# Optimization experiments

Measured on AMD Instinct MI355X. Metric: run time of the kernel, lower is better.

The kernel has to match this reference:

```python
import jax, jax.numpy as jnp
import numpy as np

N_NODES = 100000
N_EDGES = 1600000
D_IN = 128
D_OUT = 128
NEG_SLOPE = 0.01  # F.leaky_relu default

def setup_inputs() -> dict:
    key = jax.random.key(0)
    k1, k2, k3, k4, k5, k6 = jax.random.split(key, 6)
    stdv = 1.0 / np.sqrt(D_OUT)
    return {
        "node_features": jax.random.normal(k1, (N_NODES, D_IN), dtype=jnp.float32),
        "edge_row": jax.random.randint(k2, (N_EDGES,), 0, N_NODES),  # dest node per edge
        "edge_col": jax.random.randint(k3, (N_EDGES,), 0, N_NODES),  # src node per edge
        "edge_val": jax.random.uniform(k4, (N_EDGES,), dtype=jnp.float32),
        "weight": jax.random.uniform(k5, (D_IN, D_OUT), dtype=jnp.float32, minval=-stdv, maxval=stdv),
        "bias": jax.random.uniform(k6, (D_OUT,), dtype=jnp.float32, minval=-stdv, maxval=stdv),
    }

def reference(node_features, edge_row, edge_col, edge_val, weight, bias):
    # x = node_features @ W  -> [N, D_OUT]
    h = node_features @ weight
    # spmm(adj, h): gather source features, scale by edge value, scatter-add to dest
    msg = edge_val[:, None] * h[edge_col]                       # [E, D_OUT]
    out = jax.ops.segment_sum(msg, edge_row, num_segments=node_features.shape[0])
    out = out + bias
    out = jnp.where(out >= 0, out, NEG_SLOPE * out)             # leaky_relu
    # dropout p=0 -> identity
    return out
```

## Files before the change

### kernel.cpp

```cpp
#include <hip/hip_runtime.h>

#define DMODEL 128
#define NEG_SLOPE 0.01f
#define NPB 64
#define NBK_MAX 1600
#define CPAD 16
#define SBLK 256
#define CAP 1536
#define OCAP 65536

typedef unsigned int uint;
typedef unsigned short ushort_t;
typedef __attribute__((ext_vector_type(8))) short short8v;
typedef __attribute__((ext_vector_type(4))) float float4v;

__device__ inline ushort_t f2bf(float f) {
    uint u = __float_as_uint(f);
    u += 0x7FFFu + ((u >> 16) & 1u);
    return (ushort_t)(u >> 16);
}

__global__ __launch_bounds__(256) void k_pre(const float* __restrict__ W,
                                             ushort_t* __restrict__ Wt,
                                             int* __restrict__ cur,
                                             int ztot) {
    const int b = blockIdx.x;
    if (b < 64) {
        const int t = b * 256 + threadIdx.x;
        const int k = t >> 7, c = t & 127;
        Wt[(size_t)c * DMODEL + k] = f2bf(W[(size_t)k * DMODEL + c]);
    } else {
        const int i = (b - 64) * 256 + threadIdx.x;
        if (i < ztot) cur[i] = 0;
    }
}

__global__ __launch_bounds__(1024) void k_fused(
        const int* __restrict__ er, const int* __restrict__ ec,
        const float* __restrict__ ev, int* __restrict__ cur,
        int* __restrict__ ocnt, int4* __restrict__ ovf,
        int2* __restrict__ packed0, int E, int NBK, int chunk,
        const float* __restrict__ X, const ushort_t* __restrict__ Wt,
        ushort_t* __restrict__ H, int N) {
    __shared__ int lh[NBK_MAX];
    __shared__ int lb[NBK_MAX];
    const int t = threadIdx.x;

    if (blockIdx.x < SBLK) {
        for (int k = t; k < NBK; k += 1024) lh[k] = 0;
        __syncthreads();
        const int s0 = blockIdx.x * chunk;
        const int s1 = min(E, s0 + chunk);
        for (int i = s0 + t * 4; i < s1; i += 4096) {
            if (i + 3 < s1) {
                int4 r = *(const int4*)(er + i);
                atomicAdd(&lh[r.x >> 6], 1);
                atomicAdd(&lh[r.y >> 6], 1);
                atomicAdd(&lh[r.z >> 6], 1);
                atomicAdd(&lh[r.w >> 6], 1);
            } else {
                for (int q = i; q < s1; ++q) atomicAdd(&lh[er[q] >> 6], 1);
            }
        }
        __syncthreads();
        for (int k = t; k < NBK; k += 1024) {
            int c = lh[k];
            lb[k] = c ? atomicAdd(&cur[k * CPAD], c) : 0;
            lh[k] = 0;
        }
        __syncthreads();
        for (int i = s0 + t * 4; i < s1; i += 4096) {
            if (i + 3 < s1) {
                int4 r = *(const int4*)(er + i);
                int4 c = *(const int4*)(ec + i);
                float4 v = *(const float4*)(ev + i);
                int bkt, rl, slot;
#define SCAT1(RR, CC, VV)                                                     \
                bkt = (RR) >> 6; rl = (RR) & 63;                              \
                slot = lb[bkt] + atomicAdd(&lh[bkt], 1);                      \
                if (slot < CAP)                                               \
                    packed0[(size_t)bkt * CAP + slot] =                       \
                        make_int2((rl << 17) | (CC), __float_as_int(VV));     \
                else {                                                        \
                    int o = atomicAdd(ocnt, 1);                               \
                    if (o < OCAP) ovf[o] = make_int4(bkt, rl, (CC), __float_as_int(VV)); \
                }
                SCAT1(r.x, c.x, v.x)
                SCAT1(r.y, c.y, v.y)
                SCAT1(r.z, c.z, v.z)
                SCAT1(r.w, c.w, v.w)
            } else {
                for (int q = i; q < s1; ++q) {
                    int rr = er[q];
                    int bkt = rr >> 6, rl = rr & 63;
                    int slot = lb[bkt] + atomicAdd(&lh[bkt], 1);
                    if (slot < CAP)
                        packed0[(size_t)bkt * CAP + slot] =
                            make_int2((rl << 17) | ec[q], __float_as_int(ev[q]));
                    else {
                        int o = atomicAdd(ocnt, 1);
                        if (o < OCAP) ovf[o] = make_int4(bkt, rl, ec[q], __float_as_int(ev[q]));
                    }
                }
            }
        }
    } else {
        const int gb = blockIdx.x - SBLK;
        const int wid = t >> 6, lane = t & 63;
        const int wrow = (gb * 16 + wid) * 16;
        if (wrow >= N) return;
        const int lr = lane & 15;
        const int kg = lane >> 4;

        const float* xrow = X + (size_t)(wrow + lr) * DMODEL + kg * 8;
        const ushort_t* wtb = Wt + (size_t)lr * DMODEL + kg * 8;

        float4v acc[8] = {};
#pragma unroll
        for (int s = 0; s < 4; ++s) {
            float4 x0 = *(const float4*)(xrow + s * 32);
            float4 x1 = *(const float4*)(xrow + s * 32 + 4);
            short8v af;
            af[0] = (short)f2bf(x0.x); af[1] = (short)f2bf(x0.y);
            af[2] = (short)f2bf(x0.z); af[3] = (short)f2bf(x0.w);
            af[4] = (short)f2bf(x1.x); af[5] = (short)f2bf(x1.y);
            af[6] = (short)f2bf(x1.z); af[7] = (short)f2bf(x1.w);
#pragma unroll
            for (int c = 0; c < 8; ++c) {
                short8v bf = *(const short8v*)(wtb + (size_t)c * 16 * DMODEL + s * 32);
                acc[c] = __builtin_amdgcn_mfma_f32_16x16x32_bf16(af, bf, acc[c], 0, 0, 0);
            }
        }
#pragma unroll
        for (int c = 0; c < 8; ++c) {
#pragma unroll
            for (int r = 0; r < 4; ++r) {
                const int row = wrow + kg * 4 + r;
                H[(size_t)row * DMODEL + c * 16 + lr] = f2bf(acc[c][r]);
            }
        }
    }
}

__global__ __launch_bounds__(256) void k_bagg2(const uint* __restrict__ Hb,
                                               const int* __restrict__ cur,
                                               const int* __restrict__ ocnt,
                                               const int4* __restrict__ ovf,
                                               const int2* __restrict__ packed0,
                                               const float* __restrict__ bias,
                                               float* __restrict__ out, int N) {
    __shared__ int2 srt[CAP];
    __shared__ int lcnt[NPB];
    __shared__ int lpref[NPB];
    __shared__ int lcur[NPB];
    const int t = threadIdx.x;
    const int b = blockIdx.x;
    if (t < NPB) { lcnt[t] = 0; lcur[t] = 0; }
    __syncthreads();

    const int cnt = cur[b * CPAD];
    const int staged = min(cnt, CAP);
    const int2* slab = packed0 + (size_t)b * CAP;

    int2 myent[6];
#pragma unroll
    for (int k = 0; k < 6; ++k) {
        const int i = t + k * 256;
        myent[k] = make_int2(0, 0);
        if (i < staged) {
            myent[k] = slab[i];
            atomicAdd(&lcnt[((uint)myent[k].x) >> 17], 1);
        }
    }
    __syncthreads();

    if (t < NPB) {
        int p = 0;
        for (int k = 0; k < t; ++k) p += lcnt[k];
        lpref[t] = p;
    }
    __syncthreads();

#pragma unroll
    for (int k = 0; k < 6; ++k) {
        const int i = t + k * 256;
        if (i < staged) {
            const int rl = ((uint)myent[k].x) >> 17;
            const int pos = lpref[rl] + atomicAdd(&lcur[rl], 1);
            srt[pos] = make_int2(myent[k].x & 0x1FFFF, myent[k].y);
        }
    }
    __syncthreads();

    const int wid = t >> 6, lane = t & 63;
    const int h = lane >> 5, sl = lane & 31;
    const float4 bv = ((const float4*)bias)[sl];
    const int oc = min(*ocnt, OCAP);

    for (int r = wid * 16; r < wid * 16 + 16; ++r) {
        const int node = b * NPB + r;
        if (node >= N) continue;
        const int m = lcnt[r], p0 = lpref[r];
        float4 acc = make_float4(0.f, 0.f, 0.f, 0.f);
        int jj = h;
        for (; jj + 6 < m; jj += 8) {
            const int2 e0 = srt[p0 + jj];
            const int2 e1 = srt[p0 + jj + 2];
            const int2 e2 = srt[p0 + jj + 4];
            const int2 e3 = srt[p0 + jj + 6];
            const uint2 g0 = ((const uint2*)(Hb + (size_t)e0.x * 64))[sl];
            const uint2 g1 = ((const uint2*)(Hb + (size_t)e1.x * 64))[sl];
            const uint2 g2 = ((const uint2*)(Hb + (size_t)e2.x * 64))[sl];
            const uint2 g3 = ((const uint2*)(Hb + (size_t)e3.x * 64))[sl];
            const float v0 = __int_as_float(e0.y);
            const float v1 = __int_as_float(e1.y);
            const float v2 = __int_as_float(e2.y);
            const float v3 = __int_as_float(e3.y);
            acc.x = fmaf(v0, __uint_as_float(g0.x << 16), acc.x);
            acc.y = fmaf(v0, __uint_as_float(g0.x & 0xffff0000u), acc.y);
            acc.z = fmaf(v0, __uint_as_float(g0.y << 16), acc.z);
            acc.w = fmaf(v0, __uint_as_float(g0.y & 0xffff0000u), acc.w);
            acc.x = fmaf(v1, __uint_as_float(g1.x << 16), acc.x);
            acc.y = fmaf(v1, __uint_as_float(g1.x & 0xffff0000u), acc.y);
            acc.z = fmaf(v1, __uint_as_float(g1.y << 16), acc.z);
            acc.w = fmaf(v1, __uint_as_float(g1.y & 0xffff0000u), acc.w);
            acc.x = fmaf(v2, __uint_as_float(g2.x << 16), acc.x);
            acc.y = fmaf(v2, __uint_as_float(g2.x & 0xffff0000u), acc.y);
            acc.z = fmaf(v2, __uint_as_float(g2.y << 16), acc.z);
            acc.w = fmaf(v2, __uint_as_float(g2.y & 0xffff0000u), acc.w);
            acc.x = fmaf(v3, __uint_as_float(g3.x << 16), acc.x);
            acc.y = fmaf(v3, __uint_as_float(g3.x & 0xffff0000u), acc.y);
            acc.z = fmaf(v3, __uint_as_float(g3.y << 16), acc.z);
            acc.w = fmaf(v3, __uint_as_float(g3.y & 0xffff0000u), acc.w);
        }
        for (; jj < m; jj += 2) {
            const int2 e0 = srt[p0 + jj];
            const uint2 g0 = ((const uint2*)(Hb + (size_t)e0.x * 64))[sl];
            const float v0 = __int_as_float(e0.y);
            acc.x = fmaf(v0, __uint_as_float(g0.x << 16), acc.x);
            acc.y = fmaf(v0, __uint_as_float(g0.x & 0xffff0000u), acc.y);
            acc.z = fmaf(v0, __uint_as_float(g0.y << 16), acc.z);
            acc.w = fmaf(v0, __uint_as_float(g0.y & 0xffff0000u), acc.w);
        }
        for (int i = 0; i < oc; ++i) {
            const int4 o4 = ovf[i];
            if (o4.x == b && o4.y == r && h == 0) {
                const float v = __int_as_float(o4.w);
                const uint2 g = ((const uint2*)(Hb + (size_t)o4.z * 64))[sl];
                acc.x = fmaf(v, __uint_as_float(g.x << 16), acc.x);
                acc.y = fmaf(v, __uint_as_float(g.x & 0xffff0000u), acc.y);
                acc.z = fmaf(v, __uint_as_float(g.y << 16), acc.z);
                acc.w = fmaf(v, __uint_as_float(g.y & 0xffff0000u), acc.w);
            }
        }
        acc.x += __shfl_xor(acc.x, 32);
        acc.y += __shfl_xor(acc.y, 32);
        acc.z += __shfl_xor(acc.z, 32);
        acc.w += __shfl_xor(acc.w, 32);
        if (h == 0) {
            float4 o;
            o.x = acc.x + bv.x; o.y = acc.y + bv.y;
            o.z = acc.z + bv.z; o.w = acc.w + bv.w;
            o.x = o.x >= 0.f ? o.x : NEG_SLOPE * o.x;
            o.y = o.y >= 0.f ? o.y : NEG_SLOPE * o.y;
            o.z = o.z >= 0.f ? o.z : NEG_SLOPE * o.z;
            o.w = o.w >= 0.f ? o.w : NEG_SLOPE * o.w;
            ((float4*)(out + (size_t)node * DMODEL))[sl] = o;
        }
    }
}

extern "C" void kernel_launch(void* const* d_in, const int* in_sizes, int n_in,
                              void* d_out, int out_size, void* d_ws, size_t ws_size,
                              hipStream_t stream) {
    const float* X    = (const float*)d_in[0];
    const int*   er   = (const int*)d_in[1];
    const int*   ec   = (const int*)d_in[2];
    const float* ev   = (const float*)d_in[3];
    const float* W    = (const float*)d_in[4];
    const float* bias = (const float*)d_in[5];
    float* out = (float*)d_out;

    const int N = in_sizes[0] / DMODEL;
    const int E = in_sizes[1];
    const int NBK = (N + NPB - 1) / NPB;

    char* ws = (char*)d_ws;
    size_t off = 0;
    auto alloc = [&](size_t bytes) {
        void* p = ws + off;
        off += (bytes + 127) & ~(size_t)127;
        return p;
    };
    ushort_t* H   = (ushort_t*)alloc((size_t)N * DMODEL * sizeof(ushort_t));
    ushort_t* Wt  = (ushort_t*)alloc((size_t)DMODEL * DMODEL * sizeof(ushort_t));
    int* cur      = (int*)alloc(((size_t)NBK * CPAD + 1) * sizeof(int));
    int* ocnt     = cur + (size_t)NBK * CPAD;
    int4* ovf     = (int4*)alloc((size_t)OCAP * sizeof(int4));
    int2* packed0 = (int2*)alloc((size_t)NBK * CAP * sizeof(int2));
    (void)ws_size;

    const int ztot = NBK * CPAD + 1;

    hipLaunchKernelGGL(k_pre, dim3(64 + (ztot + 255) / 256), dim3(256), 0, stream,
                       W, Wt, cur, ztot);

    const int chunk = ((((E + SBLK - 1) / SBLK) + 3) & ~3);
    const int gemm_blocks = (N + 255) / 256;
    hipLaunchKernelGGL(k_fused, dim3(SBLK + gemm_blocks), dim3(1024), 0, stream,
                       er, ec, ev, cur, ocnt, ovf, packed0, E, NBK, chunk,
                       X, Wt, H, N);

    hipLaunchKernelGGL(k_bagg2, dim3(NBK), dim3(256), 0, stream,
                       (const uint*)H, cur, ocnt, ovf, packed0, bias, out, N);
}
```

Measured before the change: 149.6 us.

## Split fused scatter/GEMM kernel and stage X tile through swizzled LDS

Splits the fused kernel, which ran edge bucketing and the X@W GEMM in different blocks of one launch, into a dedicated GEMM kernel and a scatter kernel. The GEMM now uses 256-thread blocks that load a 64x128 tile of X with coalesced float4 loads, convert it to bf16 into XOR-swizzled shared memory, then feed MFMA from LDS. This is meant to replace the strided per-lane X reads and free the GEMM from the 1024-thread and large-LDS constraints of the scatter path. The cost is one more launch and no more overlap between the scatter phase and the GEMM.

Measured after the change: 149.2 us. Within noise of the previous version (-0.3%).

```diff
diff --git a/kernel.cpp b/kernel.cpp
--- a/kernel.cpp
+++ b/kernel.cpp
@@ -35,108 +35,120 @@
     }
 }
 
-__global__ __launch_bounds__(1024) void k_fused(
-        const int* __restrict__ er, const int* __restrict__ ec,
-        const float* __restrict__ ev, int* __restrict__ cur,
-        int* __restrict__ ocnt, int4* __restrict__ ovf,
-        int2* __restrict__ packed0, int E, int NBK, int chunk,
-        const float* __restrict__ X, const ushort_t* __restrict__ Wt,
-        ushort_t* __restrict__ H, int N) {
+__global__ __launch_bounds__(256) void k_gemm(const float* __restrict__ X,
+                                              const ushort_t* __restrict__ Wt,
+                                              ushort_t* __restrict__ H, int N) {
+    __shared__ ushort_t Xs[64 * 128];
+    const int t = threadIdx.x;
+    const int row0 = blockIdx.x * 64;
+
+#pragma unroll
+    for (int i = 0; i < 8; ++i) {
+        const int f = t + i * 256;
+        const int r = f >> 5;
+        const int c4 = f & 31;
+        float4 v = make_float4(0.f, 0.f, 0.f, 0.f);
+        if (row0 + r < N) v = *(const float4*)(X + (size_t)(row0 + r) * DMODEL + c4 * 4);
+        ushort4 u;
+        u.x = f2bf(v.x); u.y = f2bf(v.y); u.z = f2bf(v.z); u.w = f2bf(v.w);
+        const int chunk = (c4 >> 1) ^ (r & 7);
+        *(ushort4*)(Xs + r * 128 + chunk * 8 + (c4 & 1) * 4) = u;
+    }
+    __syncthreads();
+
+    const int wid = t >> 6, lane = t & 63;
+    const int lr = lane & 15;
+    const int kg = lane >> 4;
+    const int wr = wid * 16 + lr;
+    const ushort_t* wtb = Wt + (size_t)lr * DMODEL + kg * 8;
+
+    float4v acc[8] = {};
+#pragma unroll
+    for (int s = 0; s < 4; ++s) {
+        const int chunk = (s * 4 + kg) ^ (lr & 7);
+        const short8v af = *(const short8v*)(Xs + wr * 128 + chunk * 8);
+#pragma unroll
+        for (int c = 0; c < 8; ++c) {
+            const short8v bf = *(const short8v*)(wtb + (size_t)c * 16 * DMODEL + s * 32);
+            acc[c] = __builtin_amdgcn_mfma_f32_16x16x32_bf16(af, bf, acc[c], 0, 0, 0);
+        }
+    }
+
+#pragma unroll
+    for (int c = 0; c < 8; ++c) {
+#pragma unroll
+        for (int r = 0; r < 4; ++r) {
+            const int row = row0 + wid * 16 + kg * 4 + r;
+            if (row < N) H[(size_t)row * DMODEL + c * 16 + lr] = f2bf(acc[c][r]);
+        }
+    }
+}
+
+__global__ __launch_bounds__(1024) void k_scat(const int* __restrict__ er,
+                                               const int* __restrict__ ec,
+                                               const float* __restrict__ ev,
+                                               int* __restrict__ cur,
+                                               int* __restrict__ ocnt,
+                                               int4* __restrict__ ovf,
+                                               int2* __restrict__ packed0,
+                                               int E, int NBK, int chunk) {
     __shared__ int lh[NBK_MAX];
     __shared__ int lb[NBK_MAX];
     const int t = threadIdx.x;
-
-    if (blockIdx.x < SBLK) {
-        for (int k = t; k < NBK; k += 1024) lh[k] = 0;
-        __syncthreads();
-        const int s0 = blockIdx.x * chunk;
-        const int s1 = min(E, s0 + chunk);
-        for (int i = s0 + t * 4; i < s1; i += 4096) {
-            if (i + 3 < s1) {
-                int4 r = *(const int4*)(er + i);
-                atomicAdd(&lh[r.x >> 6], 1);
-                atomicAdd(&lh[r.y >> 6], 1);
-                atomicAdd(&lh[r.z >> 6], 1);
-                atomicAdd(&lh[r.w >> 6], 1);
-            } else {
-                for (int q = i; q < s1; ++q) atomicAdd(&lh[er[q] >> 6], 1);
+    for (int k = t; k < NBK; k += 1024) lh[k] = 0;
+    __syncthreads();
+    const int s0 = blockIdx.x * chunk;
+    const int s1 = min(E, s0 + chunk);
+    for (int i = s0 + t * 4; i < s1; i += 4096) {
+        if (i + 3 < s1) {
+            int4 r = *(const int4*)(er + i);
+            atomicAdd(&lh[r.x >> 6], 1);
+            atomicAdd(&lh[r.y >> 6], 1);
+            atomicAdd(&lh[r.z >> 6], 1);
+            atomicAdd(&lh[r.w >> 6], 1);
+        } else {
+            for (int q = i; q < s1; ++q) atomicAdd(&lh[er[q] >> 6], 1);
+        }
+    }
+    __syncthreads();
+    for (int k = t; k < NBK; k += 1024) {
+        int c = lh[k];
+        lb[k] = c ? atomicAdd(&cur[k * CPAD], c) : 0;
+        lh[k] = 0;
+    }
+    __syncthreads();
+    for (int i = s0 + t * 4; i < s1; i += 4096) {
+        if (i + 3 < s1) {
+            int4 r = *(const int4*)(er + i);
+            int4 c = *(const int4*)(ec + i);
+            float4 v = *(const float4*)(ev + i);
+            int bkt, rl, slot;
+#define SCAT1(RR, CC, VV)                                                     \
+            bkt = (RR) >> 6; rl = (RR) & 63;                                  \
+            slot = lb[bkt] + atomicAdd(&lh[bkt], 1);                          \
+            if (slot < CAP)                                                   \
+                packed0[(size_t)bkt * CAP + slot] =                           \
+                    make_int2((rl << 17) | (CC), __float_as_int(VV));         \
+            else {                                                            \
+                int o = atomicAdd(ocnt, 1);                                   \
+                if (o < OCAP) ovf[o] = make_int4(bkt, rl, (CC), __float_as_int(VV)); \
             }
-        }
-        __syncthreads();
-        for (int k = t; k < NBK; k += 1024) {
-            int c = lh[k];
-            lb[k] = c ? atomicAdd(&cur[k * CPAD], c) : 0;
-            lh[k] = 0;
-        }
-        __syncthreads();
-        for (int i = s0 + t * 4; i < s1; i += 4096) {
-            if (i + 3 < s1) {
-                int4 r = *(const int4*)(er + i);
-                int4 c = *(const int4*)(ec + i);
-                float4 v = *(const float4*)(ev + i);
-                int bkt, rl, slot;
-#define SCAT1(RR, CC, VV)                                                     \
-                bkt = (RR) >> 6; rl = (RR) & 63;                              \
-                slot = lb[bkt] + atomicAdd(&lh[bkt], 1);                      \
-                if (slot < CAP)                                               \
-                    packed0[(size_t)bkt * CAP + slot] =                       \
-                        make_int2((rl << 17) | (CC), __float_as_int(VV));     \
-                else {                                                        \
-                    int o = atomicAdd(ocnt, 1);                               \
-                    if (o < OCAP) ovf[o] = make_int4(bkt, rl, (CC), __float_as_int(VV)); \
+            SCAT1(r.x, c.x, v.x)
+            SCAT1(r.y, c.y, v.y)
+            SCAT1(r.z, c.z, v.z)
+            SCAT1(r.w, c.w, v.w)
+        } else {
+            for (int q = i; q < s1; ++q) {
+                int rr = er[q];
+                int bkt = rr >> 6, rl = rr & 63;
+                int slot = lb[bkt] + atomicAdd(&lh[bkt], 1);
+                if (slot < CAP)
+                    packed0[(size_t)bkt * CAP + slot] =
+                        make_int2((rl << 17) | ec[q], __float_as_int(ev[q]));
+                else {
+                    int o = atomicAdd(ocnt, 1);
+                    if (o < OCAP) ovf[o] = make_int4(bkt, rl, ec[q], __float_as_int(ev[q]));
                 }
-                SCAT1(r.x, c.x, v.x)
-                SCAT1(r.y, c.y, v.y)
-                SCAT1(r.z, c.z, v.z)
-                SCAT1(r.w, c.w, v.w)
-            } else {
-                for (int q = i; q < s1; ++q) {
-                    int rr = er[q];
-                    int bkt = rr >> 6, rl = rr & 63;
-                    int slot = lb[bkt] + atomicAdd(&lh[bkt], 1);
-                    if (slot < CAP)
-                        packed0[(size_t)bkt * CAP + slot] =
-                            make_int2((rl << 17) | ec[q], __float_as_int(ev[q]));
-                    else {
-                        int o = atomicAdd(ocnt, 1);
-                        if (o < OCAP) ovf[o] = make_int4(bkt, rl, ec[q], __float_as_int(ev[q]));
-                    }
-                }
-            }
-        }
-    } else {
-        const int gb = blockIdx.x - SBLK;
-        const int wid = t >> 6, lane = t & 63;
-        const int wrow = (gb * 16 + wid) * 16;
-        if (wrow >= N) return;
-        const int lr = lane & 15;
-        const int kg = lane >> 4;
-
-        const float* xrow = X + (size_t)(wrow + lr) * DMODEL + kg * 8;
-        const ushort_t* wtb = Wt + (size_t)lr * DMODEL + kg * 8;
-
-        float4v acc[8] = {};
-#pragma unroll
-        for (int s = 0; s < 4; ++s) {
-            float4 x0 = *(const float4*)(xrow + s * 32);
-            float4 x1 = *(const float4*)(xrow + s * 32 + 4);
-            short8v af;
-            af[0] = (short)f2bf(x0.x); af[1] = (short)f2bf(x0.y);
-            af[2] = (short)f2bf(x0.z); af[3] = (short)f2bf(x0.w);
-            af[4] = (short)f2bf(x1.x); af[5] = (short)f2bf(x1.y);
-            af[6] = (short)f2bf(x1.z); af[7] = (short)f2bf(x1.w);
-#pragma unroll
-            for (int c = 0; c < 8; ++c) {
-                short8v bf = *(const short8v*)(wtb + (size_t)c * 16 * DMODEL + s * 32);
-                acc[c] = __builtin_amdgcn_mfma_f32_16x16x32_bf16(af, bf, acc[c], 0, 0, 0);
-            }
-        }
-#pragma unroll
-        for (int c = 0; c < 8; ++c) {
-#pragma unroll
-            for (int r = 0; r < 4; ++r) {
-                const int row = wrow + kg * 4 + r;
-                H[(size_t)row * DMODEL + c * 16 + lr] = f2bf(acc[c][r]);
             }
         }
     }
@@ -305,11 +317,10 @@
     hipLaunchKernelGGL(k_pre, dim3(64 + (ztot + 255) / 256), dim3(256), 0, stream,
                        W, Wt, cur, ztot);
 
+    hipLaunchKernelGGL(k_gemm, dim3((N + 63) / 64), dim3(256), 0, stream, X, Wt, H, N);
     const int chunk = ((((E + SBLK - 1) / SBLK) + 3) & ~3);
-    const int gemm_blocks = (N + 255) / 256;
-    hipLaunchKernelGGL(k_fused, dim3(SBLK + gemm_blocks), dim3(1024), 0, stream,
-                       er, ec, ev, cur, ocnt, ovf, packed0, E, NBK, chunk,
-                       X, Wt, H, N);
+    hipLaunchKernelGGL(k_scat, dim3(SBLK), dim3(1024), 0, stream,
+                       er, ec, ev, cur, ocnt, ovf, packed0, E, NBK, chunk);
 
     hipLaunchKernelGGL(k_bagg2, dim3(NBK), dim3(256), 0, stream,
                        (const uint*)H, cur, ocnt, ovf, packed0, bias, out, N);
```

## Interleave smaller scatter and GEMM blocks, stage X tile in LDS, unroll gather

Applied to the files above, without the earlier changes.

The fused scatter+GEMM kernel now launches 256-thread blocks instead of 1024, with 1024 scatter blocks interleaved with GEMM blocks (odd indices scatter) so both workloads spread across CUs at once. GEMM blocks convert a 64-row X tile to bf16 into swizzled shared memory once and read MFMA A-fragments from it, replacing per-lane global loads and conversions. The aggregation kernel adds a 16-edge unrolled gather loop to keep more loads in flight. The trade-offs are more global atomics on bucket counters from the larger number of scatter blocks, and higher register pressure in the aggregation loop.

New measurement: 172.0 us. 14.9% more time.

```diff
diff --git a/kernel.cpp b/kernel.cpp
--- a/kernel.cpp
+++ b/kernel.cpp
@@ -5,7 +5,7 @@
 #define NPB 64
 #define NBK_MAX 1600
 #define CPAD 16
-#define SBLK 256
+#define NSCAT 1024
 #define CAP 1536
 #define OCAP 65536
 
@@ -35,23 +35,27 @@
     }
 }
 
-__global__ __launch_bounds__(1024) void k_fused(
+__global__ __launch_bounds__(256) void k_fused2(
         const int* __restrict__ er, const int* __restrict__ ec,
         const float* __restrict__ ev, int* __restrict__ cur,
         int* __restrict__ ocnt, int4* __restrict__ ovf,
         int2* __restrict__ packed0, int E, int NBK, int chunk,
         const float* __restrict__ X, const ushort_t* __restrict__ Wt,
         ushort_t* __restrict__ H, int N) {
-    __shared__ int lh[NBK_MAX];
-    __shared__ int lb[NBK_MAX];
+    __shared__ __align__(16) char smem[16384];
     const int t = threadIdx.x;
-
-    if (blockIdx.x < SBLK) {
-        for (int k = t; k < NBK; k += 1024) lh[k] = 0;
+    const int g = blockIdx.x;
+    const bool is_scat = (g < 2 * NSCAT) && (g & 1);
+
+    if (is_scat) {
+        int* lh = (int*)smem;
+        int* lb = lh + NBK_MAX;
+        const int sb = g >> 1;
+        for (int k = t; k < NBK; k += 256) lh[k] = 0;
         __syncthreads();
-        const int s0 = blockIdx.x * chunk;
+        const int s0 = sb * chunk;
         const int s1 = min(E, s0 + chunk);
-        for (int i = s0 + t * 4; i < s1; i += 4096) {
+        for (int i = s0 + t * 4; i < s1; i += 1024) {
             if (i + 3 < s1) {
                 int4 r = *(const int4*)(er + i);
                 atomicAdd(&lh[r.x >> 6], 1);
@@ -63,13 +67,13 @@
             }
         }
         __syncthreads();
-        for (int k = t; k < NBK; k += 1024) {
+        for (int k = t; k < NBK; k += 256) {
             int c = lh[k];
             lb[k] = c ? atomicAdd(&cur[k * CPAD], c) : 0;
             lh[k] = 0;
         }
         __syncthreads();
-        for (int i = s0 + t * 4; i < s1; i += 4096) {
+        for (int i = s0 + t * 4; i < s1; i += 1024) {
             if (i + 3 < s1) {
                 int4 r = *(const int4*)(er + i);
                 int4 c = *(const int4*)(ec + i);
@@ -105,29 +109,39 @@
             }
         }
     } else {
-        const int gb = blockIdx.x - SBLK;
+        ushort_t* Xs = (ushort_t*)smem;
+        const int idx = (g < 2 * NSCAT) ? (g >> 1) : (NSCAT + (g - 2 * NSCAT));
+        const int row0 = idx * 64;
+        if (row0 >= N) return;
+
+#pragma unroll
+        for (int i = 0; i < 8; ++i) {
+            const int f = t + i * 256;
+            const int r = f >> 5;
+            const int c4 = f & 31;
+            float4 v = make_float4(0.f, 0.f, 0.f, 0.f);
+            if (row0 + r < N) v = *(const float4*)(X + (size_t)(row0 + r) * DMODEL + c4 * 4);
+            ushort4 u;
+            u.x = f2bf(v.x); u.y = f2bf(v.y); u.z = f2bf(v.z); u.w = f2bf(v.w);
+            const int chunk16 = (c4 >> 1) ^ (r & 7);
+            *(ushort4*)(Xs + r * 128 + chunk16 * 8 + (c4 & 1) * 4) = u;
+        }
+        __syncthreads();
+
         const int wid = t >> 6, lane = t & 63;
-        const int wrow = (gb * 16 + wid) * 16;
-        if (wrow >= N) return;
         const int lr = lane & 15;
         const int kg = lane >> 4;
-
-        const float* xrow = X + (size_t)(wrow + lr) * DMODEL + kg * 8;
+        const int wr = wid * 16 + lr;
         const ushort_t* wtb = Wt + (size_t)lr * DMODEL + kg * 8;
 
         float4v acc[8] = {};
 #pragma unroll
         for (int s = 0; s < 4; ++s) {
-            float4 x0 = *(const float4*)(xrow + s * 32);
-            float4 x1 = *(const float4*)(xrow + s * 32 + 4);
-            short8v af;
-            af[0] = (short)f2bf(x0.x); af[1] = (short)f2bf(x0.y);
-            af[2] = (short)f2bf(x0.z); af[3] = (short)f2bf(x0.w);
-            af[4] = (short)f2bf(x1.x); af[5] = (short)f2bf(x1.y);
-            af[6] = (short)f2bf(x1.z); af[7] = (short)f2bf(x1.w);
+            const int chunk16 = (s * 4 + kg) ^ (lr & 7);
+            const short8v af = *(const short8v*)(Xs + wr * 128 + chunk16 * 8);
 #pragma unroll
             for (int c = 0; c < 8; ++c) {
-                short8v bf = *(const short8v*)(wtb + (size_t)c * 16 * DMODEL + s * 32);
+                const short8v bf = *(const short8v*)(wtb + (size_t)c * 16 * DMODEL + s * 32);
                 acc[c] = __builtin_amdgcn_mfma_f32_16x16x32_bf16(af, bf, acc[c], 0, 0, 0);
             }
         }
@@ -135,12 +149,21 @@
         for (int c = 0; c < 8; ++c) {
 #pragma unroll
             for (int r = 0; r < 4; ++r) {
-                const int row = wrow + kg * 4 + r;
-                H[(size_t)row * DMODEL + c * 16 + lr] = f2bf(acc[c][r]);
-            }
-        }
-    }
-}
+                const int row = row0 + wid * 16 + kg * 4 + r;
+                if (row < N) H[(size_t)row * DMODEL + c * 16 + lr] = f2bf(acc[c][r]);
+            }
+        }
+    }
+}
+
+#define EDGE_FMA(EE, GG)                                                      \
+    {                                                                         \
+        const float v_ = __int_as_float((EE).y);                              \
+        acc.x = fmaf(v_, __uint_as_float((GG).x << 16), acc.x);               \
+        acc.y = fmaf(v_, __uint_as_float((GG).x & 0xffff0000u), acc.y);       \
+        acc.z = fmaf(v_, __uint_as_float((GG).y << 16), acc.z);               \
+        acc.w = fmaf(v_, __uint_as_float((GG).y & 0xffff0000u), acc.w);       \
+    }
 
 __global__ __launch_bounds__(256) void k_bagg2(const uint* __restrict__ Hb,
                                                const int* __restrict__ cur,
@@ -203,6 +226,26 @@
         const int m = lcnt[r], p0 = lpref[r];
         float4 acc = make_float4(0.f, 0.f, 0.f, 0.f);
         int jj = h;
+        for (; jj + 14 < m; jj += 16) {
+            const int2 e0 = srt[p0 + jj];
+            const int2 e1 = srt[p0 + jj + 2];
+            const int2 e2 = srt[p0 + jj + 4];
+            const int2 e3 = srt[p0 + jj + 6];
+            const int2 e4 = srt[p0 + jj + 8];
+            const int2 e5 = srt[p0 + jj + 10];
+            const int2 e6 = srt[p0 + jj + 12];
+            const int2 e7 = srt[p0 + jj + 14];
+            const uint2 g0 = ((const uint2*)(Hb + (size_t)e0.x * 64))[sl];
+            const uint2 g1 = ((const uint2*)(Hb + (size_t)e1.x * 64))[sl];
+            const uint2 g2 = ((const uint2*)(Hb + (size_t)e2.x * 64))[sl];
+            const uint2 g3 = ((const uint2*)(Hb + (size_t)e3.x * 64))[sl];
+            const uint2 g4 = ((const uint2*)(Hb + (size_t)e4.x * 64))[sl];
+            const uint2 g5 = ((const uint2*)(Hb + (size_t)e5.x * 64))[sl];
+            const uint2 g6 = ((const uint2*)(Hb + (size_t)e6.x * 64))[sl];
+            const uint2 g7 = ((const uint2*)(Hb + (size_t)e7.x * 64))[sl];
+            EDGE_FMA(e0, g0) EDGE_FMA(e1, g1) EDGE_FMA(e2, g2) EDGE_FMA(e3, g3)
+            EDGE_FMA(e4, g4) EDGE_FMA(e5, g5) EDGE_FMA(e6, g6) EDGE_FMA(e7, g7)
+        }
         for (; jj + 6 < m; jj += 8) {
             const int2 e0 = srt[p0 + jj];
             const int2 e1 = srt[p0 + jj + 2];
@@ -212,35 +255,12 @@
             const uint2 g1 = ((const uint2*)(Hb + (size_t)e1.x * 64))[sl];
             const uint2 g2 = ((const uint2*)(Hb + (size_t)e2.x * 64))[sl];
             const uint2 g3 = ((const uint2*)(Hb + (size_t)e3.x * 64))[sl];
-            const float v0 = __int_as_float(e0.y);
-            const float v1 = __int_as_float(e1.y);
-            const float v2 = __int_as_float(e2.y);
-            const float v3 = __int_as_float(e3.y);
-            acc.x = fmaf(v0, __uint_as_float(g0.x << 16), acc.x);
-            acc.y = fmaf(v0, __uint_as_float(g0.x & 0xffff0000u), acc.y);
-            acc.z = fmaf(v0, __uint_as_float(g0.y << 16), acc.z);
-            acc.w = fmaf(v0, __uint_as_float(g0.y & 0xffff0000u), acc.w);
-            acc.x = fmaf(v1, __uint_as_float(g1.x << 16), acc.x);
-            acc.y = fmaf(v1, __uint_as_float(g1.x & 0xffff0000u), acc.y);
-            acc.z = fmaf(v1, __uint_as_float(g1.y << 16), acc.z);
-            acc.w = fmaf(v1, __uint_as_float(g1.y & 0xffff0000u), acc.w);
-            acc.x = fmaf(v2, __uint_as_float(g2.x << 16), acc.x);
-            acc.y = fmaf(v2, __uint_as_float(g2.x & 0xffff0000u), acc.y);
-            acc.z = fmaf(v2, __uint_as_float(g2.y << 16), acc.z);
-            acc.w = fmaf(v2, __uint_as_float(g2.y & 0xffff0000u), acc.w);
-            acc.x = fmaf(v3, __uint_as_float(g3.x << 16), acc.x);
-            acc.y = fmaf(v3, __uint_as_float(g3.x & 0xffff0000u), acc.y);
-            acc.z = fmaf(v3, __uint_as_float(g3.y << 16), acc.z);
-            acc.w = fmaf(v3, __uint_as_float(g3.y & 0xffff0000u), acc.w);
+            EDGE_FMA(e0, g0) EDGE_FMA(e1, g1) EDGE_FMA(e2, g2) EDGE_FMA(e3, g3)
         }
         for (; jj < m; jj += 2) {
             const int2 e0 = srt[p0 + jj];
             const uint2 g0 = ((const uint2*)(Hb + (size_t)e0.x * 64))[sl];
-            const float v0 = __int_as_float(e0.y);
-            acc.x = fmaf(v0, __uint_as_float(g0.x << 16), acc.x);
-            acc.y = fmaf(v0, __uint_as_float(g0.x & 0xffff0000u), acc.y);
-            acc.z = fmaf(v0, __uint_as_float(g0.y << 16), acc.z);
-            acc.w = fmaf(v0, __uint_as_float(g0.y & 0xffff0000u), acc.w);
+            EDGE_FMA(e0, g0)
         }
         for (int i = 0; i < oc; ++i) {
             const int4 o4 = ovf[i];
@@ -305,9 +325,10 @@
     hipLaunchKernelGGL(k_pre, dim3(64 + (ztot + 255) / 256), dim3(256), 0, stream,
                        W, Wt, cur, ztot);
 
-    const int chunk = ((((E + SBLK - 1) / SBLK) + 3) & ~3);
-    const int gemm_blocks = (N + 255) / 256;
-    hipLaunchKernelGGL(k_fused, dim3(SBLK + gemm_blocks), dim3(1024), 0, stream,
+    const int GB = (N + 63) / 64;
+    const int chunk = ((((E + NSCAT - 1) / NSCAT) + 3) & ~3);
+    const int total = NSCAT + GB;
+    hipLaunchKernelGGL(k_fused2, dim3(total), dim3(256), 0, stream,
                        er, ec, ev, cur, ocnt, ovf, packed0, E, NBK, chunk,
                        X, Wt, H, N);
 
```
